# Kernel tuning notes

Hardware: AMD Instinct MI355X
Metric: run time of the kernel (lower is better)

Reference implementation:

```python
import jax, jax.numpy as jnp
import numpy as np

E = 1024
H = 16
DFF = 4 * E
EPS = 1e-5


def layer_norm(x, scale, bias):
    mu = jnp.mean(x, axis=-1, keepdims=True)
    var = jnp.var(x, axis=-1, keepdims=True)
    return (x - mu) * jax.lax.rsqrt(var + EPS) * scale + bias


def setup_inputs() -> dict:
    key = jax.random.key(0)
    ks = jax.random.split(key, 12)
    N, L = 2, 2048
    x = jax.random.normal(ks[0], (N, L, E), dtype=jnp.float32)
    attn_mask = jax.random.randint(ks[1], (N, H, L, L), 0, 2) == 1
    s = 0.02
    return {
        "x": x,
        "attn_mask": attn_mask,
        "ln1_s": jnp.ones((E,), jnp.float32),
        "ln1_b": jnp.zeros((E,), jnp.float32),
        "Wqkv": jax.random.normal(ks[2], (E, 3 * E), jnp.float32) * s,
        "bqkv": jnp.zeros((3 * E,), jnp.float32),
        "Wo": jax.random.normal(ks[3], (E, E), jnp.float32) * s,
        "bo": jnp.zeros((E,), jnp.float32),
        "ln2_s": jnp.ones((E,), jnp.float32),
        "ln2_b": jnp.zeros((E,), jnp.float32),
        "lnf_s": jnp.ones((E,), jnp.float32),
        "lnf_b": jnp.zeros((E,), jnp.float32),
        "W1": jax.random.normal(ks[4], (E, DFF), jnp.float32) * s,
        "b1": jnp.zeros((DFF,), jnp.float32),
        "W2": jax.random.normal(ks[5], (DFF, E), jnp.float32) * s,
        "b2": jnp.zeros((E,), jnp.float32),
    }


def reference(x, attn_mask, ln1_s, ln1_b, Wqkv, bqkv, Wo, bo,
              ln2_s, ln2_b, lnf_s, lnf_b, W1, b1, W2, b2):
    N, L, _ = x.shape
    D = E // H
    # --- self attention (pre-norm) ---
    h = layer_norm(x, ln1_s, ln1_b)
    qkv = h @ Wqkv + bqkv                      # [N,L,3E]
    q, k, v = jnp.split(qkv, 3, axis=-1)
    q = q.reshape(N, L, H, D)
    k = k.reshape(N, L, H, D)
    v = v.reshape(N, L, H, D)
    a = jnp.einsum('nqhd,nkhd->nhqk', q, k) * (D ** -0.5)  # [N,H,L,L]
    a = jnp.where(attn_mask, -jnp.inf, a)
    a = jax.nn.softmax(a, axis=-1)
    o = jnp.einsum('nhqk,nkhd->nqhd', a, v).reshape(N, L, E)
    o = o @ Wo + bo
    x = x + o
    # --- feedforward (norm_2 then FF's internal LN) ---
    h = layer_norm(x, ln2_s, ln2_b)
    h = layer_norm(h, lnf_s, lnf_b)
    h = jax.nn.gelu(h @ W1 + b1, approximate=False) @ W2 + b2
    return x + h
```

## Files before the change

kernel.cpp:

```cpp
#include <hip/hip_runtime.h>
#include <math.h>

#define E_DIM 1024
#define H_HEADS 16
#define D_HEAD 64
#define DFF_DIM 4096
#define L_SEQ 2048
#define N_BATCH 2
#define T_TOK (N_BATCH * L_SEQ)
#define HT64 ((size_t)H_HEADS * T_TOK * 64)

typedef __attribute__((ext_vector_type(8))) __bf16 bf16x8;
typedef __attribute__((ext_vector_type(4))) float f32x4;

__device__ __forceinline__ unsigned short f2bf(float f) {
  union { float f; unsigned int u; } v; v.f = f;
  unsigned int r = v.u + 0x7fffu + ((v.u >> 16) & 1u);
  return (unsigned short)(r >> 16);
}

__device__ __forceinline__ void gl2lds16(const void* g, void* l) {
  __builtin_amdgcn_global_load_lds(
      (const __attribute__((address_space(1))) unsigned int*)g,
      (__attribute__((address_space(3))) unsigned int*)l, 16, 0, 0);
}

__global__ __launch_bounds__(256) void convert_transpose(
    const float* __restrict__ in, unsigned short* __restrict__ out, int K, int N) {
  __shared__ float tile[32][33];
  int n0 = blockIdx.x * 32, k0 = blockIdx.y * 32;
  int tx = threadIdx.x & 31, ty = threadIdx.x >> 5;
#pragma unroll
  for (int i = 0; i < 32; i += 8)
    tile[ty + i][tx] = in[(size_t)(k0 + ty + i) * N + n0 + tx];
  __syncthreads();
#pragma unroll
  for (int i = 0; i < 32; i += 8)
    out[(size_t)(n0 + ty + i) * K + k0 + tx] = f2bf(tile[tx][ty + i]);
}

__device__ __forceinline__ void block_reduce2(float& a, float& b, float* sm, int tid) {
#pragma unroll
  for (int off = 32; off > 0; off >>= 1) {
    a += __shfl_down(a, off);
    b += __shfl_down(b, off);
  }
  int wid = tid >> 6;
  if ((tid & 63) == 0) { sm[wid * 2] = a; sm[wid * 2 + 1] = b; }
  __syncthreads();
  a = sm[0] + sm[2] + sm[4] + sm[6];
  b = sm[1] + sm[3] + sm[5] + sm[7];
}

__global__ __launch_bounds__(256) void ln_kernel(
    const float* __restrict__ x, const float* __restrict__ s,
    const float* __restrict__ b, unsigned short* __restrict__ out) {
  int row = blockIdx.x, tid = threadIdx.x;
  __shared__ float sm[8];
  float4 v = ((const float4*)(x + (size_t)row * E_DIM))[tid];
  float sum = v.x + v.y + v.z + v.w;
  float sq = v.x * v.x + v.y * v.y + v.z * v.z + v.w * v.w;
  block_reduce2(sum, sq, sm, tid);
  float mu = sum * (1.0f / E_DIM);
  float var = sq * (1.0f / E_DIM) - mu * mu;
  float rs = rsqrtf(var + 1e-5f);
  float4 sv = ((const float4*)s)[tid];
  float4 bv = ((const float4*)b)[tid];
  ushort4 o4;
  o4.x = f2bf((v.x - mu) * rs * sv.x + bv.x);
  o4.y = f2bf((v.y - mu) * rs * sv.y + bv.y);
  o4.z = f2bf((v.z - mu) * rs * sv.z + bv.z);
  o4.w = f2bf((v.w - mu) * rs * sv.w + bv.w);
  ((ushort4*)(out + (size_t)row * E_DIM))[tid] = o4;
}

__global__ __launch_bounds__(256) void ln2_kernel(
    const float* __restrict__ x, const float* __restrict__ s2,
    const float* __restrict__ b2, const float* __restrict__ sf,
    const float* __restrict__ bf_, unsigned short* __restrict__ out) {
  int row = blockIdx.x, tid = threadIdx.x;
  __shared__ float sm[8];
  float4 v = ((const float4*)(x + (size_t)row * E_DIM))[tid];
  float sum = v.x + v.y + v.z + v.w;
  float sq = v.x * v.x + v.y * v.y + v.z * v.z + v.w * v.w;
  block_reduce2(sum, sq, sm, tid);
  float mu = sum * (1.0f / E_DIM);
  float rs = rsqrtf(sq * (1.0f / E_DIM) - mu * mu + 1e-5f);
  float4 s2v = ((const float4*)s2)[tid];
  float4 b2v = ((const float4*)b2)[tid];
  float y0 = (v.x - mu) * rs * s2v.x + b2v.x;
  float y1 = (v.y - mu) * rs * s2v.y + b2v.y;
  float y2 = (v.z - mu) * rs * s2v.z + b2v.z;
  float y3 = (v.w - mu) * rs * s2v.w + b2v.w;
  float sum2 = y0 + y1 + y2 + y3;
  float sq2 = y0 * y0 + y1 * y1 + y2 * y2 + y3 * y3;
  __syncthreads();
  block_reduce2(sum2, sq2, sm, tid);
  float mu2 = sum2 * (1.0f / E_DIM);
  float rs2 = rsqrtf(sq2 * (1.0f / E_DIM) - mu2 * mu2 + 1e-5f);
  float4 sfv = ((const float4*)sf)[tid];
  float4 bfv = ((const float4*)bf_)[tid];
  ushort4 o4;
  o4.x = f2bf((y0 - mu2) * rs2 * sfv.x + bfv.x);
  o4.y = f2bf((y1 - mu2) * rs2 * sfv.y + bfv.y);
  o4.z = f2bf((y2 - mu2) * rs2 * sfv.z + bfv.z);
  o4.w = f2bf((y3 - mu2) * rs2 * sfv.w + bfv.w);
  ((ushort4*)(out + (size_t)row * E_DIM))[tid] = o4;
}

__device__ __forceinline__ float gelu_exact(float v) {
  float z = v * 0.70710678118f;
  float az = fabsf(z);
  float t = 1.0f / (1.0f + 0.3275911f * az);
  float poly = ((((1.061405429f * t - 1.453152027f) * t + 1.421413741f) * t -
                 0.284496736f) * t + 0.254829592f) * t;
  float y = 1.0f - poly * __expf(-az * az);
  float er = (z < 0.0f) ? -y : y;
  return 0.5f * v * (1.0f + er);
}

template <int EPI>
__global__ __launch_bounds__(256) void gemm_bt(
    const unsigned short* __restrict__ A, const unsigned short* __restrict__ Bt,
    const float* __restrict__ bias, const float* __restrict__ resid,
    void* __restrict__ outp, int M, int N, int K) {
  __shared__ unsigned short As[128 * 32];
  __shared__ unsigned short Bs[128 * 32];
  int tid = threadIdx.x;
  int lane = tid & 63, wave = tid >> 6;
  int m0 = blockIdx.y * 128, n0 = blockIdx.x * 128;
  int wm = (wave & 1) * 64, wn = (wave >> 1) * 64;
  int lm = lane & 15, lq = lane >> 4;

  int r0 = tid >> 2, coff = (tid & 3) * 8;
  const unsigned short* Abase = A + (size_t)m0 * K;
  const unsigned short* Bbase = Bt + (size_t)n0 * K;
  unsigned short* lA0 = As + wave * 512;
  unsigned short* lA1 = As + 2048 + wave * 512;
  unsigned short* lB0 = Bs + wave * 512;
  unsigned short* lB1 = Bs + 2048 + wave * 512;

  f32x4 acc[4][4] = {};
  for (int k0 = 0; k0 < K; k0 += 32) {
    __syncthreads();
    gl2lds16(Abase + (size_t)r0 * K + k0 + coff, lA0);
    gl2lds16(Abase + (size_t)(r0 + 64) * K + k0 + coff, lA1);
    gl2lds16(Bbase + (size_t)r0 * K + k0 + coff, lB0);
    gl2lds16(Bbase + (size_t)(r0 + 64) * K + k0 + coff, lB1);
    __syncthreads();
    bf16x8 a[4], b[4];
#pragma unroll
    for (int i = 0; i < 4; i++)
      a[i] = *(const bf16x8*)(As + (wm + i * 16 + lm) * 32 + lq * 8);
#pragma unroll
    for (int j = 0; j < 4; j++)
      b[j] = *(const bf16x8*)(Bs + (wn + j * 16 + lm) * 32 + lq * 8);
#pragma unroll
    for (int i = 0; i < 4; i++)
#pragma unroll
      for (int j = 0; j < 4; j++)
        acc[i][j] = __builtin_amdgcn_mfma_f32_16x16x32_bf16(a[i], b[j], acc[i][j], 0, 0, 0);
  }
#pragma unroll
  for (int i = 0; i < 4; i++)
#pragma unroll
    for (int j = 0; j < 4; j++) {
      int row = m0 + wm + i * 16 + lq * 4;
      int col = n0 + wn + j * 16 + lm;
      float bcol = bias[col];
#pragma unroll
      for (int r = 0; r < 4; r++) {
        float v = acc[i][j][r] + bcol;
        if (EPI == 0) {
          ((unsigned short*)outp)[(size_t)(row + r) * N + col] = f2bf(v);
        } else if (EPI == 1) {
          ((unsigned short*)outp)[(size_t)(row + r) * N + col] = f2bf(gelu_exact(v));
        } else if (EPI == 2) {
          size_t idx = (size_t)(row + r) * N + col;
          ((float*)outp)[idx] = resid[idx] + v;
        } else {
          int which = col >> 10, hh = (col & 1023) >> 6, d = col & 63;
          unsigned short* dst = (unsigned short*)outp + (size_t)which * HT64 +
                                ((size_t)hh * T_TOK + row + r) * 64 + d;
          *dst = f2bf(v);
        }
      }
    }
}

__global__ __launch_bounds__(256) void attn_kernel(
    const unsigned short* __restrict__ qkvh, const int* __restrict__ mask,
    unsigned short* __restrict__ o) {
  const int bq = blockIdx.x;
  const int nh = blockIdx.y;
  const int h = nh & 15;
  const int tid = threadIdx.x, lane = tid & 63, wave = tid >> 6;
  const int lm = lane & 15, lq = lane >> 4;

  __shared__ unsigned short Ks[64 * 72];
  __shared__ unsigned short Vt[64 * 72];
  __shared__ unsigned short Ps[4][16 * 72];
  __shared__ unsigned int Msk[64 * 17];

  const int q_base = bq * 64;
  const int tok0 = (nh >> 4) * L_SEQ;
  const unsigned short* qh = qkvh + (size_t)h * T_TOK * 64;
  const unsigned short* kh = qkvh + HT64 + (size_t)h * T_TOK * 64;
  const unsigned short* vh = qkvh + 2 * HT64 + (size_t)h * T_TOK * 64;
  const int* mbase = mask + (size_t)nh * L_SEQ * L_SEQ;

  bf16x8 qf[2];
  {
    int t = tok0 + q_base + wave * 16 + lm;
    qf[0] = *(const bf16x8*)(qh + (size_t)t * 64 + lq * 8);
    qf[1] = *(const bf16x8*)(qh + (size_t)t * 64 + 32 + lq * 8);
  }

  const int skey = tid >> 3, schunk = tid & 7;
  const int mq0 = (tid >> 4) * 4, mkc = tid & 15;
  const int qrow = q_base + wave * 16 + lq * 4;

  float m_run[4], l_run[4];
  f32x4 oacc[4] = {};
#pragma unroll
  for (int r = 0; r < 4; r++) { m_run[r] = -1e30f; l_run[r] = 0.0f; }

  for (int kt = 0; kt < L_SEQ / 64; kt++) {
    const int k_base = kt * 64;
    const int t0 = tok0 + k_base;
    uint4 kv0 = *(const uint4*)(kh + (size_t)(t0 + skey) * 64 + schunk * 8);
    uint4 kv1 = *(const uint4*)(kh + (size_t)(t0 + skey + 32) * 64 + schunk * 8);
    uint4 vv0 = *(const uint4*)(vh + (size_t)(t0 + skey) * 64 + schunk * 8);
    uint4 vv1 = *(const uint4*)(vh + (size_t)(t0 + skey + 32) * 64 + schunk * 8);
    const int* mrow = mbase + (size_t)(q_base + mq0) * L_SEQ + k_base + mkc * 4;
    int4 mr0 = *(const int4*)(mrow);
    int4 mr1 = *(const int4*)(mrow + L_SEQ);
    int4 mr2 = *(const int4*)(mrow + 2 * L_SEQ);
    int4 mr3 = *(const int4*)(mrow + 3 * L_SEQ);
    __syncthreads();
    *(uint4*)(Ks + skey * 72 + schunk * 8) = kv0;
    *(uint4*)(Ks + (skey + 32) * 72 + schunk * 8) = kv1;
    {
      const unsigned short* p0 = (const unsigned short*)&vv0;
      const unsigned short* p1 = (const unsigned short*)&vv1;
#pragma unroll
      for (int jj = 0; jj < 8; jj++) {
        int jx = (jj + schunk) & 7;
        Vt[(schunk * 8 + jx) * 72 + skey] = p0[jx];
        Vt[(schunk * 8 + jx) * 72 + skey + 32] = p1[jx];
      }
    }
    {
      const int* a0 = (const int*)&mr0;
      const int* a1 = (const int*)&mr1;
      const int* a2 = (const int*)&mr2;
      const int* a3 = (const int*)&mr3;
#pragma unroll
      for (int kk = 0; kk < 4; kk++) {
        unsigned u = (a0[kk] ? 1u : 0u) | (a1[kk] ? 256u : 0u) |
                     (a2[kk] ? 65536u : 0u) | (a3[kk] ? 16777216u : 0u);
        Msk[(mkc * 4 + kk) * 17 + (mq0 >> 2)] = u;
      }
    }
    __syncthreads();

    f32x4 s[4];
#pragma unroll
    for (int nt = 0; nt < 4; nt++) {
      int key = nt * 16 + lm;
      bf16x8 kb0 = *(const bf16x8*)(Ks + key * 72 + lq * 8);
      bf16x8 kb1 = *(const bf16x8*)(Ks + key * 72 + 32 + lq * 8);
      f32x4 acc = {};
      acc = __builtin_amdgcn_mfma_f32_16x16x32_bf16(qf[0], kb0, acc, 0, 0, 0);
      acc = __builtin_amdgcn_mfma_f32_16x16x32_bf16(qf[1], kb1, acc, 0, 0, 0);
      s[nt] = acc;
    }
#pragma unroll
    for (int nt = 0; nt < 4; nt++) {
      unsigned mu = Msk[(nt * 16 + lm) * 17 + wave * 4 + lq];
#pragma unroll
      for (int r = 0; r < 4; r++) {
        float v = s[nt][r] * 0.125f;
        s[nt][r] = ((mu >> (8 * r)) & 0xffu) ? -1e30f : v;
      }
    }
    float alpha[4], rsum[4];
#pragma unroll
    for (int r = 0; r < 4; r++) {
      float v = fmaxf(fmaxf(s[0][r], s[1][r]), fmaxf(s[2][r], s[3][r]));
#pragma unroll
      for (int mo = 1; mo < 16; mo <<= 1) v = fmaxf(v, __shfl_xor(v, mo));
      float mn = fmaxf(m_run[r], v);
      alpha[r] = __expf(m_run[r] - mn);
      m_run[r] = mn;
      rsum[r] = 0.0f;
    }
    unsigned short* pw = Ps[wave];
#pragma unroll
    for (int nt = 0; nt < 4; nt++)
#pragma unroll
      for (int r = 0; r < 4; r++) {
        float p = __expf(s[nt][r] - m_run[r]);
        rsum[r] += p;
        pw[(lq * 4 + r) * 72 + nt * 16 + lm] = f2bf(p);
      }
#pragma unroll
    for (int r = 0; r < 4; r++) {
      float v = rsum[r];
#pragma unroll
      for (int mo = 1; mo < 16; mo <<= 1) v += __shfl_xor(v, mo);
      l_run[r] = l_run[r] * alpha[r] + v;
    }
#pragma unroll
    for (int j = 0; j < 4; j++)
#pragma unroll
      for (int r = 0; r < 4; r++) oacc[j][r] *= alpha[r];
    __syncthreads();

#pragma unroll
    for (int c = 0; c < 2; c++) {
      bf16x8 pa = *(const bf16x8*)(pw + lm * 72 + c * 32 + lq * 8);
#pragma unroll
      for (int j = 0; j < 4; j++) {
        bf16x8 vb = *(const bf16x8*)(Vt + (j * 16 + lm) * 72 + c * 32 + lq * 8);
        oacc[j] = __builtin_amdgcn_mfma_f32_16x16x32_bf16(pa, vb, oacc[j], 0, 0, 0);
      }
    }
  }
#pragma unroll
  for (int r = 0; r < 4; r++) {
    float inv_l = 1.0f / l_run[r];
    int t = tok0 + qrow + r;
#pragma unroll
    for (int j = 0; j < 4; j++)
      o[(size_t)t * E_DIM + h * 64 + j * 16 + lm] = f2bf(oacc[j][r] * inv_l);
  }
}

extern "C" void kernel_launch(void* const* d_in, const int* in_sizes, int n_in,
                              void* d_out, int out_size, void* d_ws, size_t ws_size,
                              hipStream_t stream) {
  const float* x = (const float*)d_in[0];
  const int* mask = (const int*)d_in[1];
  const float* ln1_s = (const float*)d_in[2];
  const float* ln1_b = (const float*)d_in[3];
  const float* Wqkv = (const float*)d_in[4];
  const float* bqkv = (const float*)d_in[5];
  const float* Wo = (const float*)d_in[6];
  const float* bo = (const float*)d_in[7];
  const float* ln2_s = (const float*)d_in[8];
  const float* ln2_b = (const float*)d_in[9];
  const float* lnf_s = (const float*)d_in[10];
  const float* lnf_b = (const float*)d_in[11];
  const float* W1 = (const float*)d_in[12];
  const float* b1 = (const float*)d_in[13];
  const float* W2 = (const float*)d_in[14];
  const float* b2 = (const float*)d_in[15];

  size_t off = 0;
  auto alloc = [&](size_t bytes) {
    void* p = (char*)d_ws + off;
    off += (bytes + 255) & ~(size_t)255;
    return p;
  };
  unsigned short* WqkvT = (unsigned short*)alloc((size_t)3072 * 1024 * 2);
  unsigned short* WoT = (unsigned short*)alloc((size_t)1024 * 1024 * 2);
  unsigned short* W1T = (unsigned short*)alloc((size_t)4096 * 1024 * 2);
  unsigned short* W2T = (unsigned short*)alloc((size_t)1024 * 4096 * 2);
  unsigned short* h1 = (unsigned short*)alloc((size_t)T_TOK * E_DIM * 2);
  unsigned short* qkvh = (unsigned short*)alloc(3 * HT64 * 2);
  unsigned short* ob = (unsigned short*)alloc((size_t)T_TOK * E_DIM * 2);
  float* x2 = (float*)alloc((size_t)T_TOK * E_DIM * 4);
  unsigned short* h2 = (unsigned short*)alloc((size_t)T_TOK * E_DIM * 2);
  unsigned short* g1 = (unsigned short*)alloc((size_t)T_TOK * DFF_DIM * 2);

  convert_transpose<<<dim3(3072 / 32, 1024 / 32), 256, 0, stream>>>(Wqkv, WqkvT, 1024, 3072);
  convert_transpose<<<dim3(1024 / 32, 1024 / 32), 256, 0, stream>>>(Wo, WoT, 1024, 1024);
  convert_transpose<<<dim3(4096 / 32, 1024 / 32), 256, 0, stream>>>(W1, W1T, 1024, 4096);
  convert_transpose<<<dim3(1024 / 32, 4096 / 32), 256, 0, stream>>>(W2, W2T, 4096, 1024);
  ln_kernel<<<T_TOK, 256, 0, stream>>>(x, ln1_s, ln1_b, h1);
  gemm_bt<3><<<dim3(3072 / 128, T_TOK / 128), 256, 0, stream>>>(
      h1, WqkvT, bqkv, nullptr, qkvh, T_TOK, 3072, 1024);
  attn_kernel<<<dim3(L_SEQ / 64, N_BATCH * H_HEADS), 256, 0, stream>>>(qkvh, mask, ob);
  gemm_bt<2><<<dim3(1024 / 128, T_TOK / 128), 256, 0, stream>>>(
      ob, WoT, bo, x, x2, T_TOK, 1024, 1024);
  ln2_kernel<<<T_TOK, 256, 0, stream>>>(x2, ln2_s, ln2_b, lnf_s, lnf_b, h2);
  gemm_bt<1><<<dim3(DFF_DIM / 128, T_TOK / 128), 256, 0, stream>>>(
      h2, W1T, b1, nullptr, g1, T_TOK, DFF_DIM, 1024);
  gemm_bt<2><<<dim3(1024 / 128, T_TOK / 128), 256, 0, stream>>>(
      g1, W2T, b2, x2, (float*)d_out, T_TOK, 1024, 4096);

  (void)in_sizes; (void)n_in; (void)out_size; (void)ws_size;
}
```

Measured before the change: 1.164 ms.

## Split-K final FFN GEMM with atomics, prefetch attention tiles, merge weight converts

The final W2 GEMM is split four ways along K using grid z. Each slice atomically adds its partial sums into the output, which ln2_kernel pre-initializes with the residual plus bias; this raises the block count for a GEMM that otherwise launches only 256 blocks. The attention kernel now issues the next tile's K, V and mask global loads right after the LDS barrier so they overlap with the current tile's compute. The four weight convert/transpose launches are merged into one kernel. The risks are fp32 atomic contention, nondeterministic summation order, and extra register pressure in attention.

```diff
diff --git a/kernel.cpp b/kernel.cpp
--- a/kernel.cpp
+++ b/kernel.cpp
@@ -25,18 +25,28 @@
       (__attribute__((address_space(3))) unsigned int*)l, 16, 0, 0);
 }
 
-__global__ __launch_bounds__(256) void convert_transpose(
-    const float* __restrict__ in, unsigned short* __restrict__ out, int K, int N) {
-  __shared__ float tile[32][33];
-  int n0 = blockIdx.x * 32, k0 = blockIdx.y * 32;
+__global__ __launch_bounds__(256) void convert_all(
+    const float* __restrict__ Wqkv, const float* __restrict__ Wo,
+    const float* __restrict__ W1, const float* __restrict__ W2,
+    unsigned short* __restrict__ o0, unsigned short* __restrict__ o1,
+    unsigned short* __restrict__ o2, unsigned short* __restrict__ o3) {
+  int b = blockIdx.x;
+  const float* in; unsigned short* out; int K, N, tile;
+  if (b < 3072)      { in = Wqkv; out = o0; K = 1024; N = 3072; tile = b; }
+  else if (b < 4096) { in = Wo;   out = o1; K = 1024; N = 1024; tile = b - 3072; }
+  else if (b < 8192) { in = W1;   out = o2; K = 1024; N = 4096; tile = b - 4096; }
+  else               { in = W2;   out = o3; K = 4096; N = 1024; tile = b - 8192; }
+  int ntx = N >> 5;
+  int n0 = (tile % ntx) * 32, k0 = (tile / ntx) * 32;
+  __shared__ float tilebuf[32][33];
   int tx = threadIdx.x & 31, ty = threadIdx.x >> 5;
 #pragma unroll
   for (int i = 0; i < 32; i += 8)
-    tile[ty + i][tx] = in[(size_t)(k0 + ty + i) * N + n0 + tx];
+    tilebuf[ty + i][tx] = in[(size_t)(k0 + ty + i) * N + n0 + tx];
   __syncthreads();
 #pragma unroll
   for (int i = 0; i < 32; i += 8)
-    out[(size_t)(n0 + ty + i) * K + k0 + tx] = f2bf(tile[tx][ty + i]);
+    out[(size_t)(n0 + ty + i) * K + k0 + tx] = f2bf(tilebuf[tx][ty + i]);
 }
 
 __device__ __forceinline__ void block_reduce2(float& a, float& b, float* sm, int tid) {
@@ -77,10 +87,17 @@
 __global__ __launch_bounds__(256) void ln2_kernel(
     const float* __restrict__ x, const float* __restrict__ s2,
     const float* __restrict__ b2, const float* __restrict__ sf,
-    const float* __restrict__ bf_, unsigned short* __restrict__ out) {
+    const float* __restrict__ bf_, unsigned short* __restrict__ out,
+    const float* __restrict__ b2ff, float* __restrict__ out_init) {
   int row = blockIdx.x, tid = threadIdx.x;
   __shared__ float sm[8];
   float4 v = ((const float4*)(x + (size_t)row * E_DIM))[tid];
+  {
+    float4 bb = ((const float4*)b2ff)[tid];
+    float4 oi;
+    oi.x = v.x + bb.x; oi.y = v.y + bb.y; oi.z = v.z + bb.z; oi.w = v.w + bb.w;
+    ((float4*)(out_init + (size_t)row * E_DIM))[tid] = oi;
+  }
   float sum = v.x + v.y + v.z + v.w;
   float sq = v.x * v.x + v.y * v.y + v.z * v.z + v.w * v.w;
   block_reduce2(sum, sq, sm, tid);
@@ -140,8 +157,11 @@
   unsigned short* lB0 = Bs + wave * 512;
   unsigned short* lB1 = Bs + 2048 + wave * 512;
 
+  int ks = K / gridDim.z;
+  int kb = ks * blockIdx.z;
+
   f32x4 acc[4][4] = {};
-  for (int k0 = 0; k0 < K; k0 += 32) {
+  for (int k0 = kb; k0 < kb + ks; k0 += 32) {
     __syncthreads();
     gl2lds16(Abase + (size_t)r0 * K + k0 + coff, lA0);
     gl2lds16(Abase + (size_t)(r0 + 64) * K + k0 + coff, lA1);
@@ -167,7 +187,7 @@
     for (int j = 0; j < 4; j++) {
       int row = m0 + wm + i * 16 + lq * 4;
       int col = n0 + wn + j * 16 + lm;
-      float bcol = bias[col];
+      float bcol = (EPI == 4) ? 0.0f : bias[col];
 #pragma unroll
       for (int r = 0; r < 4; r++) {
         float v = acc[i][j][r] + bcol;
@@ -178,11 +198,13 @@
         } else if (EPI == 2) {
           size_t idx = (size_t)(row + r) * N + col;
           ((float*)outp)[idx] = resid[idx] + v;
-        } else {
+        } else if (EPI == 3) {
           int which = col >> 10, hh = (col & 1023) >> 6, d = col & 63;
           unsigned short* dst = (unsigned short*)outp + (size_t)which * HT64 +
                                 ((size_t)hh * T_TOK + row + r) * 64 + d;
           *dst = f2bf(v);
+        } else {
+          atomicAdd((float*)outp + (size_t)(row + r) * N + col, v);
         }
       }
     }
@@ -219,24 +241,29 @@
   const int skey = tid >> 3, schunk = tid & 7;
   const int mq0 = (tid >> 4) * 4, mkc = tid & 15;
   const int qrow = q_base + wave * 16 + lq * 4;
+  const int* mcol = mbase + (size_t)(q_base + mq0) * L_SEQ + mkc * 4;
 
   float m_run[4], l_run[4];
   f32x4 oacc[4] = {};
 #pragma unroll
   for (int r = 0; r < 4; r++) { m_run[r] = -1e30f; l_run[r] = 0.0f; }
 
-  for (int kt = 0; kt < L_SEQ / 64; kt++) {
-    const int k_base = kt * 64;
-    const int t0 = tok0 + k_base;
-    uint4 kv0 = *(const uint4*)(kh + (size_t)(t0 + skey) * 64 + schunk * 8);
-    uint4 kv1 = *(const uint4*)(kh + (size_t)(t0 + skey + 32) * 64 + schunk * 8);
-    uint4 vv0 = *(const uint4*)(vh + (size_t)(t0 + skey) * 64 + schunk * 8);
-    uint4 vv1 = *(const uint4*)(vh + (size_t)(t0 + skey + 32) * 64 + schunk * 8);
-    const int* mrow = mbase + (size_t)(q_base + mq0) * L_SEQ + k_base + mkc * 4;
-    int4 mr0 = *(const int4*)(mrow);
-    int4 mr1 = *(const int4*)(mrow + L_SEQ);
-    int4 mr2 = *(const int4*)(mrow + 2 * L_SEQ);
-    int4 mr3 = *(const int4*)(mrow + 3 * L_SEQ);
+  uint4 kv0, kv1, vv0, vv1;
+  int4 mr0, mr1, mr2, mr3;
+  {
+    const int t0 = tok0;
+    kv0 = *(const uint4*)(kh + (size_t)(t0 + skey) * 64 + schunk * 8);
+    kv1 = *(const uint4*)(kh + (size_t)(t0 + skey + 32) * 64 + schunk * 8);
+    vv0 = *(const uint4*)(vh + (size_t)(t0 + skey) * 64 + schunk * 8);
+    vv1 = *(const uint4*)(vh + (size_t)(t0 + skey + 32) * 64 + schunk * 8);
+    mr0 = *(const int4*)(mcol);
+    mr1 = *(const int4*)(mcol + L_SEQ);
+    mr2 = *(const int4*)(mcol + 2 * L_SEQ);
+    mr3 = *(const int4*)(mcol + 3 * L_SEQ);
+  }
+
+  const int NT = L_SEQ / 64;
+  for (int kt = 0; kt < NT; kt++) {
     __syncthreads();
     *(uint4*)(Ks + skey * 72 + schunk * 8) = kv0;
     *(uint4*)(Ks + (skey + 32) * 72 + schunk * 8) = kv1;
@@ -263,6 +290,19 @@
       }
     }
     __syncthreads();
+
+    if (kt + 1 < NT) {
+      const int t1 = tok0 + (kt + 1) * 64;
+      kv0 = *(const uint4*)(kh + (size_t)(t1 + skey) * 64 + schunk * 8);
+      kv1 = *(const uint4*)(kh + (size_t)(t1 + skey + 32) * 64 + schunk * 8);
+      vv0 = *(const uint4*)(vh + (size_t)(t1 + skey) * 64 + schunk * 8);
+      vv1 = *(const uint4*)(vh + (size_t)(t1 + skey + 32) * 64 + schunk * 8);
+      const int* mrow = mcol + (size_t)(kt + 1) * 64;
+      mr0 = *(const int4*)(mrow);
+      mr1 = *(const int4*)(mrow + L_SEQ);
+      mr2 = *(const int4*)(mrow + 2 * L_SEQ);
+      mr3 = *(const int4*)(mrow + 3 * L_SEQ);
+    }
 
     f32x4 s[4];
 #pragma unroll
@@ -374,21 +414,19 @@
   unsigned short* h2 = (unsigned short*)alloc((size_t)T_TOK * E_DIM * 2);
   unsigned short* g1 = (unsigned short*)alloc((size_t)T_TOK * DFF_DIM * 2);
 
-  convert_transpose<<<dim3(3072 / 32, 1024 / 32), 256, 0, stream>>>(Wqkv, WqkvT, 1024, 3072);
-  convert_transpose<<<dim3(1024 / 32, 1024 / 32), 256, 0, stream>>>(Wo, WoT, 1024, 1024);
-  convert_transpose<<<dim3(4096 / 32, 1024 / 32), 256, 0, stream>>>(W1, W1T, 1024, 4096);
-  convert_transpose<<<dim3(1024 / 32, 4096 / 32), 256, 0, stream>>>(W2, W2T, 4096, 1024);
+  convert_all<<<12288, 256, 0, stream>>>(Wqkv, Wo, W1, W2, WqkvT, WoT, W1T, W2T);
   ln_kernel<<<T_TOK, 256, 0, stream>>>(x, ln1_s, ln1_b, h1);
   gemm_bt<3><<<dim3(3072 / 128, T_TOK / 128), 256, 0, stream>>>(
       h1, WqkvT, bqkv, nullptr, qkvh, T_TOK, 3072, 1024);
   attn_kernel<<<dim3(L_SEQ / 64, N_BATCH * H_HEADS), 256, 0, stream>>>(qkvh, mask, ob);
   gemm_bt<2><<<dim3(1024 / 128, T_TOK / 128), 256, 0, stream>>>(
       ob, WoT, bo, x, x2, T_TOK, 1024, 1024);
-  ln2_kernel<<<T_TOK, 256, 0, stream>>>(x2, ln2_s, ln2_b, lnf_s, lnf_b, h2);
+  ln2_kernel<<<T_TOK, 256, 0, stream>>>(x2, ln2_s, ln2_b, lnf_s, lnf_b, h2,
+                                        b2, (float*)d_out);
   gemm_bt<1><<<dim3(DFF_DIM / 128, T_TOK / 128), 256, 0, stream>>>(
       h2, W1T, b1, nullptr, g1, T_TOK, DFF_DIM, 1024);
-  gemm_bt<2><<<dim3(1024 / 128, T_TOK / 128), 256, 0, stream>>>(
-      g1, W2T, b2, x2, (float*)d_out, T_TOK, 1024, 4096);
+  gemm_bt<4><<<dim3(1024 / 128, T_TOK / 128, 4), 256, 0, stream>>>(
+      g1, W2T, nullptr, nullptr, (float*)d_out, T_TOK, 1024, 4096);
 
   (void)in_sizes; (void)n_in; (void)out_size; (void)ws_size;
 }
```

After: 1.114 ms. 4.2% less time.
